# Optimization experiments

Measured on AMD Instinct MI355X. Metric: run time of the kernel, lower is better.

## Reference

```python
import jax, jax.numpy as jnp
import numpy as np

WIN, SIGMA = 11, 1.5
C1, C2, EPS = 0.01 ** 2, 0.03 ** 2, 1e-8


def _gauss_window(win=WIN, sigma=SIGMA):
    coords = jnp.arange(win, dtype=jnp.float32) - (win - 1) / 2
    g = jnp.exp(-coords ** 2 / (2 * sigma ** 2))
    g = g / g.sum()
    return (g[:, None] * g[None, :])[None, None, :, :]


def setup_inputs() -> dict:
    key = jax.random.key(0)
    k1, k2 = jax.random.split(key)
    N, C, H, W = 32, 1, 512, 512
    x = jax.random.uniform(k1, (N, C, H, W), dtype=jnp.float32)
    y = jax.random.uniform(k2, (N, C, H, W), dtype=jnp.float32)
    w = _gauss_window()
    return {"x": x, "y": y, "w": w}


def _conv(x, w):
    pad = w.shape[-1] // 2
    return jax.lax.conv_general_dilated(
        x, w, window_strides=(1, 1), padding=[(pad, pad), (pad, pad)],
        dimension_numbers=("NCHW", "OIHW", "NCHW"))


def reference(x, y, w):
    w = w.astype(x.dtype)
    n = x.shape[0]
    # One fused conv over all five planes stacked on the batch dim.
    stacked = jnp.concatenate([x, y, x * x, y * y, x * y], axis=0)
    conv = _conv(stacked, w)
    mu_x, mu_y, ex2, ey2, exy = (conv[i * n:(i + 1) * n] for i in range(5))
    mu_x2, mu_y2, mu_xy = mu_x ** 2, mu_y ** 2, mu_x * mu_y
    sig_x2 = ex2 - mu_x2
    sig_y2 = ey2 - mu_y2
    sig_xy = exy - mu_xy
    num = (2 * mu_xy + C1) * (2 * sig_xy + C2)
    den = (mu_x2 + mu_y2 + C1) * (sig_x2 + sig_y2 + C2)
    return jnp.clip(num / (den + EPS), 0.0, 1.0).mean()
```

## Files before the change

### kernel.cpp

```cpp
#include <hip/hip_runtime.h>


#define IMG_H 512
#define IMG_W 512
#define NIMG  32
#define TW    128
#define RROWS 64
#define NBANDS (IMG_W / TW)
#define NCHUNK (IMG_H / RROWS)

#define C1F  1.0e-4f
#define C2F  9.0e-4f
#define EPSF 1.0e-8f

__global__ __launch_bounds__(TW) void ssim_kernel(
    const float* __restrict__ xg, const float* __restrict__ yg,
    const float* __restrict__ wg, float* __restrict__ out)
{
    const int t     = threadIdx.x;
    const int band  = blockIdx.x;
    const int chunk = blockIdx.y;
    const int img   = blockIdx.z;
    const int c0 = band * TW;
    const int r0 = chunk * RROWS;
    const float* xb = xg + (size_t)img * (IMG_H * IMG_W);
    const float* yb = yg + (size_t)img * (IMG_H * IMG_W);

    __shared__ float gS[11];
    __shared__ float bufX[2][TW + 16];
    __shared__ float bufY[2][TW + 16];
    __shared__ float wredS[2];

    if (t < 11) {
        float s = 0.f;
        #pragma unroll
        for (int j = 0; j < 11; ++j) s += wg[t * 11 + j];
        gS[t] = s;
    }
    __syncthreads();
    float g[11];
    #pragma unroll
    for (int k = 0; k < 11; ++k) g[k] = gS[k];

    const int colA = c0 + t;
    const int  b2     = (t < 5) ? t : (TW + t);
    const int  colB   = c0 - 5 + b2;
    const bool hasB   = (t < 10);
    const bool colBok = hasB && ((unsigned)colB < IMG_W);

    float vx[11], vy[11], vs[11], vd[11];

    {
        int rcur = r0 - 5;
        bool rok = ((unsigned)rcur < IMG_H);
        (void)rok;
    }
    float lxA, lyA, lxB, lyB;
    {
        int rcur = r0 - 5;
        bool rv = ((unsigned)rcur < IMG_H);
        const float* xr = xb + rcur * IMG_W;
        const float* yr = yb + rcur * IMG_W;
        lxA = rv ? xr[colA] : 0.f;
        lyA = rv ? yr[colA] : 0.f;
        lxB = (rv && colBok) ? xr[colB] : 0.f;
        lyB = (rv && colBok) ? yr[colB] : 0.f;
    }

    float acc = 0.f;

    for (int ii = 0; ii < 77; ii += 11) {
        #pragma unroll
        for (int s = 0; s < 11; ++s) {
            const int i = ii + s;
            if (i < RROWS + 10) {
                const int pb = i & 1;
                bufX[pb][5 + t] = lxA;
                bufY[pb][5 + t] = lyA;
                if (hasB) {
                    bufX[pb][b2] = lxB;
                    bufY[pb][b2] = lyB;
                }
                __syncthreads();

                {
                    int rn = r0 - 4 + i;
                    bool rv = ((unsigned)rn < IMG_H);
                    const float* xr = xb + rn * IMG_W;
                    const float* yr = yb + rn * IMG_W;
                    lxA = rv ? xr[colA] : 0.f;
                    lyA = rv ? yr[colA] : 0.f;
                    lxB = (rv && colBok) ? xr[colB] : 0.f;
                    lyB = (rv && colBok) ? yr[colB] : 0.f;
                }

                float hx = 0.f, hy = 0.f, hs2 = 0.f, hd2 = 0.f;
                #pragma unroll
                for (int k = 0; k < 11; ++k) {
                    float xv = bufX[pb][t + k];
                    float yv = bufY[pb][t + k];
                    hx = fmaf(g[k], xv, hx);
                    hy = fmaf(g[k], yv, hy);
                    float sv = xv + yv;
                    float dv = xv - yv;
                    hs2 = fmaf(g[k], sv * sv, hs2);
                    hd2 = fmaf(g[k], dv * dv, hd2);
                }
                vx[s] = hx; vy[s] = hy; vs[s] = hs2; vd[s] = hd2;

                if (i >= 10) {
                    float mx = 0.f, my = 0.f, ms = 0.f, md = 0.f;
                    #pragma unroll
                    for (int j = 0; j < 11; ++j) {
                        const int sl = (s + 1 + j) % 11;
                        mx = fmaf(g[j], vx[sl], mx);
                        my = fmaf(g[j], vy[sl], my);
                        ms = fmaf(g[j], vs[sl], ms);
                        md = fmaf(g[j], vd[sl], md);
                    }
                    float mux2 = mx * mx, muy2 = my * my, muxy = mx * my;
                    float a    = mux2 + muy2;
                    float esum = 0.5f  * (ms + md);
                    float exy  = 0.25f * (ms - md);
                    float sxy  = exy  - muxy;
                    float ssum = esum - a;
                    float num  = fmaf(2.f, muxy, C1F) * fmaf(2.f, sxy, C2F);
                    float den  = (a + C1F) * (ssum + C2F);
                    float v = num * __builtin_amdgcn_rcpf(den + EPSF);
                    v = fminf(fmaxf(v, 0.f), 1.f);
                    acc += v;
                }
            }
        }
    }

    #pragma unroll
    for (int off = 32; off > 0; off >>= 1)
        acc += __shfl_down(acc, off, 64);
    if ((t & 63) == 0) wredS[t >> 6] = acc;
    __syncthreads();
    if (t == 0) {
        float tot = wredS[0] + wredS[1];
        atomicAdd(out, tot * (1.0f / (float)((size_t)NIMG * IMG_H * IMG_W)));
    }
}

extern "C" void kernel_launch(void* const* d_in, const int* in_sizes, int n_in,
                              void* d_out, int out_size, void* d_ws, size_t ws_size,
                              hipStream_t stream) {
    const float* x = (const float*)d_in[0];
    const float* y = (const float*)d_in[1];
    const float* w = (const float*)d_in[2];
    float* out = (float*)d_out;

    hipMemsetAsync(out, 0, sizeof(float), stream);

    dim3 grid(NBANDS, NCHUNK, NIMG);
    ssim_kernel<<<grid, dim3(TW), 0, stream>>>(x, y, w, out);
}
```

Measured before the change: 136.3 us.

## Compute four output columns per lane with float4 register windows, drop shared memory

Each 64-lane block now handles a 256-column band over 16 rows. Each lane computes four adjacent outputs from a 20-float register window it loads directly with float4 reads, so the LDS staging and per-row __syncthreads are gone. The second-moment planes become x²+y² and xy instead of (x+y)² and (x−y)², which saves the 0.5/0.25 rescale. The costs are redundant halo loads (5 float4 per lane for 4 outputs), much higher register pressure from 11x4x4 row buffers, and smaller row chunks, so a larger share of each block's reads are halo rows.

```diff
diff --git a/kernel.cpp b/kernel.cpp
--- a/kernel.cpp
+++ b/kernel.cpp
@@ -4,131 +4,125 @@
 #define IMG_H 512
 #define IMG_W 512
 #define NIMG  32
-#define TW    128
-#define RROWS 64
-#define NBANDS (IMG_W / TW)
-#define NCHUNK (IMG_H / RROWS)
+#define M     4
+#define RROWS 16
+#define ITERS (RROWS + 10)
+#define NB4   (IMG_W / 4)
 
 #define C1F  1.0e-4f
 #define C2F  9.0e-4f
 #define EPSF 1.0e-8f
 
-__global__ __launch_bounds__(TW) void ssim_kernel(
+__global__ __launch_bounds__(64, 2) void ssim_kernel(
     const float* __restrict__ xg, const float* __restrict__ yg,
     const float* __restrict__ wg, float* __restrict__ out)
 {
-    const int t     = threadIdx.x;
-    const int band  = blockIdx.x;
-    const int chunk = blockIdx.y;
-    const int img   = blockIdx.z;
-    const int c0 = band * TW;
-    const int r0 = chunk * RROWS;
+    const int lane = threadIdx.x;
+    const int band = blockIdx.x;
+    const int chnk = blockIdx.y;
+    const int img  = blockIdx.z;
+    const int r0   = chnk * RROWS;
+    const int fb0  = band * 64 + lane - 2;
+
     const float* xb = xg + (size_t)img * (IMG_H * IMG_W);
     const float* yb = yg + (size_t)img * (IMG_H * IMG_W);
 
-    __shared__ float gS[11];
-    __shared__ float bufX[2][TW + 16];
-    __shared__ float bufY[2][TW + 16];
-    __shared__ float wredS[2];
-
-    if (t < 11) {
-        float s = 0.f;
+    float rs = 0.f;
+    if (lane < 11) {
         #pragma unroll
-        for (int j = 0; j < 11; ++j) s += wg[t * 11 + j];
-        gS[t] = s;
+        for (int j = 0; j < 11; ++j) rs += wg[lane * 11 + j];
     }
-    __syncthreads();
     float g[11];
     #pragma unroll
-    for (int k = 0; k < 11; ++k) g[k] = gS[k];
-
-    const int colA = c0 + t;
-    const int  b2     = (t < 5) ? t : (TW + t);
-    const int  colB   = c0 - 5 + b2;
-    const bool hasB   = (t < 10);
-    const bool colBok = hasB && ((unsigned)colB < IMG_W);
-
-    float vx[11], vy[11], vs[11], vd[11];
-
-    {
-        int rcur = r0 - 5;
-        bool rok = ((unsigned)rcur < IMG_H);
-        (void)rok;
-    }
-    float lxA, lyA, lxB, lyB;
-    {
-        int rcur = r0 - 5;
-        bool rv = ((unsigned)rcur < IMG_H);
-        const float* xr = xb + rcur * IMG_W;
-        const float* yr = yb + rcur * IMG_W;
-        lxA = rv ? xr[colA] : 0.f;
-        lyA = rv ? yr[colA] : 0.f;
-        lxB = (rv && colBok) ? xr[colB] : 0.f;
-        lyB = (rv && colBok) ? yr[colB] : 0.f;
+    for (int k = 0; k < 11; ++k) {
+        int gi = __shfl(__float_as_int(rs), k, 64);
+        g[k] = __int_as_float(__builtin_amdgcn_readfirstlane(gi));
     }
 
+    float rx[11][M], ry[11][M], rp[11][M], rq[11][M];
+
+    const float4 z4 = make_float4(0.f, 0.f, 0.f, 0.f);
     float acc = 0.f;
 
-    for (int ii = 0; ii < 77; ii += 11) {
+    for (int ii = 0; ii < 33; ii += 11) {
         #pragma unroll
         for (int s = 0; s < 11; ++s) {
             const int i = ii + s;
-            if (i < RROWS + 10) {
-                const int pb = i & 1;
-                bufX[pb][5 + t] = lxA;
-                bufY[pb][5 + t] = lyA;
-                if (hasB) {
-                    bufX[pb][b2] = lxB;
-                    bufY[pb][b2] = lyB;
-                }
-                __syncthreads();
-
-                {
-                    int rn = r0 - 4 + i;
-                    bool rv = ((unsigned)rn < IMG_H);
-                    const float* xr = xb + rn * IMG_W;
-                    const float* yr = yb + rn * IMG_W;
-                    lxA = rv ? xr[colA] : 0.f;
-                    lyA = rv ? yr[colA] : 0.f;
-                    lxB = (rv && colBok) ? xr[colB] : 0.f;
-                    lyB = (rv && colBok) ? yr[colB] : 0.f;
+            if (i < ITERS) {
+                const int r = r0 - 5 + i;
+                float4 xv[5], yv[5];
+                if ((unsigned)r < IMG_H) {
+                    const float4* xr4 = (const float4*)(xb + (size_t)r * IMG_W);
+                    const float4* yr4 = (const float4*)(yb + (size_t)r * IMG_W);
+                    #pragma unroll
+                    for (int k = 0; k < 5; ++k) {
+                        const int fb = fb0 + k;
+                        const bool ok = ((unsigned)fb < NB4);
+                        xv[k] = ok ? xr4[fb] : z4;
+                        yv[k] = ok ? yr4[fb] : z4;
+                    }
+                } else {
+                    #pragma unroll
+                    for (int k = 0; k < 5; ++k) { xv[k] = z4; yv[k] = z4; }
                 }
 
-                float hx = 0.f, hy = 0.f, hs2 = 0.f, hd2 = 0.f;
+                float xw[20], yw[20];
                 #pragma unroll
-                for (int k = 0; k < 11; ++k) {
-                    float xv = bufX[pb][t + k];
-                    float yv = bufY[pb][t + k];
-                    hx = fmaf(g[k], xv, hx);
-                    hy = fmaf(g[k], yv, hy);
-                    float sv = xv + yv;
-                    float dv = xv - yv;
-                    hs2 = fmaf(g[k], sv * sv, hs2);
-                    hd2 = fmaf(g[k], dv * dv, hd2);
+                for (int k = 0; k < 5; ++k) {
+                    xw[4*k+0] = xv[k].x; xw[4*k+1] = xv[k].y;
+                    xw[4*k+2] = xv[k].z; xw[4*k+3] = xv[k].w;
+                    yw[4*k+0] = yv[k].x; yw[4*k+1] = yv[k].y;
+                    yw[4*k+2] = yv[k].z; yw[4*k+3] = yv[k].w;
                 }
-                vx[s] = hx; vy[s] = hy; vs[s] = hs2; vd[s] = hd2;
+
+                float hx[M] = {0,0,0,0}, hy[M] = {0,0,0,0};
+                float hp[M] = {0,0,0,0}, hq[M] = {0,0,0,0};
+                #pragma unroll
+                for (int e = 3; e <= 16; ++e) {
+                    const float xe = xw[e], ye = yw[e];
+                    const float pe = fmaf(xe, xe, ye * ye);
+                    const float qe = xe * ye;
+                    const int jlo = (e - 13 > 0) ? (e - 13) : 0;
+                    const int jhi = (e - 3 < M - 1) ? (e - 3) : (M - 1);
+                    #pragma unroll
+                    for (int j = jlo; j <= jhi; ++j) {
+                        const float gk = g[e - 3 - j];
+                        hx[j] = fmaf(gk, xe, hx[j]);
+                        hy[j] = fmaf(gk, ye, hy[j]);
+                        hp[j] = fmaf(gk, pe, hp[j]);
+                        hq[j] = fmaf(gk, qe, hq[j]);
+                    }
+                }
+                #pragma unroll
+                for (int j = 0; j < M; ++j) {
+                    rx[s][j] = hx[j]; ry[s][j] = hy[j];
+                    rp[s][j] = hp[j]; rq[s][j] = hq[j];
+                }
 
                 if (i >= 10) {
-                    float mx = 0.f, my = 0.f, ms = 0.f, md = 0.f;
                     #pragma unroll
-                    for (int j = 0; j < 11; ++j) {
-                        const int sl = (s + 1 + j) % 11;
-                        mx = fmaf(g[j], vx[sl], mx);
-                        my = fmaf(g[j], vy[sl], my);
-                        ms = fmaf(g[j], vs[sl], ms);
-                        md = fmaf(g[j], vd[sl], md);
+                    for (int j = 0; j < M; ++j) {
+                        float mx = 0.f, my = 0.f, mp = 0.f, mq = 0.f;
+                        #pragma unroll
+                        for (int t = 0; t < 11; ++t) {
+                            const int sl = (s + 1 + t) % 11;
+                            mx = fmaf(g[t], rx[sl][j], mx);
+                            my = fmaf(g[t], ry[sl][j], my);
+                            mp = fmaf(g[t], rp[sl][j], mp);
+                            mq = fmaf(g[t], rq[sl][j], mq);
+                        }
+                        const float mux2 = mx * mx;
+                        const float muy2 = my * my;
+                        const float muxy = mx * my;
+                        const float a    = mux2 + muy2;
+                        const float sxy  = mq - muxy;
+                        const float ssum = mp - a;
+                        const float num  = fmaf(2.f, muxy, C1F) * fmaf(2.f, sxy, C2F);
+                        const float den  = (a + C1F) * (ssum + C2F);
+                        float v = num * __builtin_amdgcn_rcpf(den + EPSF);
+                        v = fminf(fmaxf(v, 0.f), 1.f);
+                        acc += v;
                     }
-                    float mux2 = mx * mx, muy2 = my * my, muxy = mx * my;
-                    float a    = mux2 + muy2;
-                    float esum = 0.5f  * (ms + md);
-                    float exy  = 0.25f * (ms - md);
-                    float sxy  = exy  - muxy;
-                    float ssum = esum - a;
-                    float num  = fmaf(2.f, muxy, C1F) * fmaf(2.f, sxy, C2F);
-                    float den  = (a + C1F) * (ssum + C2F);
-                    float v = num * __builtin_amdgcn_rcpf(den + EPSF);
-                    v = fminf(fmaxf(v, 0.f), 1.f);
-                    acc += v;
                 }
             }
         }
@@ -137,12 +131,8 @@
     #pragma unroll
     for (int off = 32; off > 0; off >>= 1)
         acc += __shfl_down(acc, off, 64);
-    if ((t & 63) == 0) wredS[t >> 6] = acc;
-    __syncthreads();
-    if (t == 0) {
-        float tot = wredS[0] + wredS[1];
-        atomicAdd(out, tot * (1.0f / (float)((size_t)NIMG * IMG_H * IMG_W)));
-    }
+    if (lane == 0)
+        atomicAdd(out, acc * (1.0f / (float)((size_t)NIMG * IMG_H * IMG_W)));
 }
 
 extern "C" void kernel_launch(void* const* d_in, const int* in_sizes, int n_in,
@@ -155,6 +145,6 @@
 
     hipMemsetAsync(out, 0, sizeof(float), stream);
 
-    dim3 grid(NBANDS, NCHUNK, NIMG);
-    ssim_kernel<<<grid, dim3(TW), 0, stream>>>(x, y, w, out);
+    dim3 grid(IMG_W / (64 * M), IMG_H / RROWS, NIMG);
+    ssim_kernel<<<grid, dim3(64), 0, stream>>>(x, y, w, out);
 }
```

Result: slower. 179.7 us (+31.9%).

## Precompute per-pixel products into float4 LDS and halve row chunk size

Applied to the files above, without the earlier changes.

Each pixel is now staged once in shared memory as a float4 holding x, y, x²+y² and x·y. The horizontal pass then does a single vector LDS read and four FMAs per tap, instead of two scalar reads plus recomputing sum and difference squares at every tap. The row chunk per block is cut from 64 to 32, which doubles the grid and the parallelism but raises the halo-row overhead from 10/64 to 10/32. Gaussian weights are now shared with wave shuffles instead of a shared-memory write and barrier, and an extra barrier is added before the final reduction.

```diff
diff --git a/kernel.cpp b/kernel.cpp
--- a/kernel.cpp
+++ b/kernel.cpp
@@ -5,9 +5,9 @@
 #define IMG_W 512
 #define NIMG  32
 #define TW    128
-#define RROWS 64
-#define NBANDS (IMG_W / TW)
-#define NCHUNK (IMG_H / RROWS)
+#define RROWS 32
+#define ITERS (RROWS + 10)
+#define LDSW  (TW + 10)
 
 #define C1F  1.0e-4f
 #define C2F  9.0e-4f
@@ -17,30 +17,33 @@
     const float* __restrict__ xg, const float* __restrict__ yg,
     const float* __restrict__ wg, float* __restrict__ out)
 {
-    const int t     = threadIdx.x;
-    const int band  = blockIdx.x;
-    const int chunk = blockIdx.y;
-    const int img   = blockIdx.z;
-    const int c0 = band * TW;
-    const int r0 = chunk * RROWS;
+    const int t    = threadIdx.x;
+    const int band = blockIdx.x;
+    const int chnk = blockIdx.y;
+    const int img  = blockIdx.z;
+    const int c0   = band * TW;
+    const int r0   = chnk * RROWS;
+
     const float* xb = xg + (size_t)img * (IMG_H * IMG_W);
     const float* yb = yg + (size_t)img * (IMG_H * IMG_W);
 
-    __shared__ float gS[11];
-    __shared__ float bufX[2][TW + 16];
-    __shared__ float bufY[2][TW + 16];
+    __shared__ float4 sq[2][LDSW];
     __shared__ float wredS[2];
 
-    if (t < 11) {
-        float s = 0.f;
-        #pragma unroll
-        for (int j = 0; j < 11; ++j) s += wg[t * 11 + j];
-        gS[t] = s;
+    float rs = 0.f;
+    {
+        const int lane = t & 63;
+        if (lane < 11) {
+            #pragma unroll
+            for (int j = 0; j < 11; ++j) rs += wg[lane * 11 + j];
+        }
     }
-    __syncthreads();
     float g[11];
     #pragma unroll
-    for (int k = 0; k < 11; ++k) g[k] = gS[k];
+    for (int k = 0; k < 11; ++k) {
+        int gi = __shfl(__float_as_int(rs), k, 64);
+        g[k] = __int_as_float(__builtin_amdgcn_readfirstlane(gi));
+    }
 
     const int colA = c0 + t;
     const int  b2     = (t < 5) ? t : (TW + t);
@@ -48,19 +51,14 @@
     const bool hasB   = (t < 10);
     const bool colBok = hasB && ((unsigned)colB < IMG_W);
 
-    float vx[11], vy[11], vs[11], vd[11];
+    float rx[11], ry[11], rp[11], rq[11];
 
-    {
-        int rcur = r0 - 5;
-        bool rok = ((unsigned)rcur < IMG_H);
-        (void)rok;
-    }
     float lxA, lyA, lxB, lyB;
     {
-        int rcur = r0 - 5;
-        bool rv = ((unsigned)rcur < IMG_H);
-        const float* xr = xb + rcur * IMG_W;
-        const float* yr = yb + rcur * IMG_W;
+        const int r = r0 - 5;
+        const bool rv = ((unsigned)r < IMG_H);
+        const float* xr = xb + (size_t)r * IMG_W;
+        const float* yr = yb + (size_t)r * IMG_W;
         lxA = rv ? xr[colA] : 0.f;
         lyA = rv ? yr[colA] : 0.f;
         lxB = (rv && colBok) ? xr[colB] : 0.f;
@@ -69,66 +67,69 @@
 
     float acc = 0.f;
 
-    for (int ii = 0; ii < 77; ii += 11) {
+    for (int ii = 0; ii < 44; ii += 11) {
         #pragma unroll
         for (int s = 0; s < 11; ++s) {
             const int i = ii + s;
-            if (i < RROWS + 10) {
+            if (i < ITERS) {
                 const int pb = i & 1;
-                bufX[pb][5 + t] = lxA;
-                bufY[pb][5 + t] = lyA;
-                if (hasB) {
-                    bufX[pb][b2] = lxB;
-                    bufY[pb][b2] = lyB;
+                {
+                    float4 v;
+                    v.x = lxA; v.y = lyA;
+                    v.z = fmaf(lxA, lxA, lyA * lyA);
+                    v.w = lxA * lyA;
+                    sq[pb][5 + t] = v;
+                    if (hasB) {
+                        float4 h;
+                        h.x = lxB; h.y = lyB;
+                        h.z = fmaf(lxB, lxB, lyB * lyB);
+                        h.w = lxB * lyB;
+                        sq[pb][b2] = h;
+                    }
                 }
                 __syncthreads();
 
                 {
-                    int rn = r0 - 4 + i;
-                    bool rv = ((unsigned)rn < IMG_H);
-                    const float* xr = xb + rn * IMG_W;
-                    const float* yr = yb + rn * IMG_W;
+                    const int r = r0 - 4 + i;
+                    const bool rv = ((unsigned)r < IMG_H);
+                    const float* xr = xb + (size_t)r * IMG_W;
+                    const float* yr = yb + (size_t)r * IMG_W;
                     lxA = rv ? xr[colA] : 0.f;
                     lyA = rv ? yr[colA] : 0.f;
                     lxB = (rv && colBok) ? xr[colB] : 0.f;
                     lyB = (rv && colBok) ? yr[colB] : 0.f;
                 }
 
-                float hx = 0.f, hy = 0.f, hs2 = 0.f, hd2 = 0.f;
+                float hx = 0.f, hy = 0.f, hp = 0.f, hq = 0.f;
                 #pragma unroll
                 for (int k = 0; k < 11; ++k) {
-                    float xv = bufX[pb][t + k];
-                    float yv = bufY[pb][t + k];
-                    hx = fmaf(g[k], xv, hx);
-                    hy = fmaf(g[k], yv, hy);
-                    float sv = xv + yv;
-                    float dv = xv - yv;
-                    hs2 = fmaf(g[k], sv * sv, hs2);
-                    hd2 = fmaf(g[k], dv * dv, hd2);
+                    const float4 w = sq[pb][t + k];
+                    hx = fmaf(g[k], w.x, hx);
+                    hy = fmaf(g[k], w.y, hy);
+                    hp = fmaf(g[k], w.z, hp);
+                    hq = fmaf(g[k], w.w, hq);
                 }
-                vx[s] = hx; vy[s] = hy; vs[s] = hs2; vd[s] = hd2;
+                rx[s] = hx; ry[s] = hy; rp[s] = hp; rq[s] = hq;
 
                 if (i >= 10) {
-                    float mx = 0.f, my = 0.f, ms = 0.f, md = 0.f;
+                    float mx = 0.f, my = 0.f, mp = 0.f, mq = 0.f;
                     #pragma unroll
                     for (int j = 0; j < 11; ++j) {
                         const int sl = (s + 1 + j) % 11;
-                        mx = fmaf(g[j], vx[sl], mx);
-                        my = fmaf(g[j], vy[sl], my);
-                        ms = fmaf(g[j], vs[sl], ms);
-                        md = fmaf(g[j], vd[sl], md);
+                        mx = fmaf(g[j], rx[sl], mx);
+                        my = fmaf(g[j], ry[sl], my);
+                        mp = fmaf(g[j], rp[sl], mp);
+                        mq = fmaf(g[j], rq[sl], mq);
                     }
-                    float mux2 = mx * mx, muy2 = my * my, muxy = mx * my;
-                    float a    = mux2 + muy2;
-                    float esum = 0.5f  * (ms + md);
-                    float exy  = 0.25f * (ms - md);
-                    float sxy  = exy  - muxy;
-                    float ssum = esum - a;
-                    float num  = fmaf(2.f, muxy, C1F) * fmaf(2.f, sxy, C2F);
-                    float den  = (a + C1F) * (ssum + C2F);
+                    const float mux2 = mx * mx, muy2 = my * my;
+                    const float muxy = mx * my;
+                    const float a    = mux2 + muy2;
+                    const float sxy  = mq - muxy;
+                    const float ssum = mp - a;
+                    const float num  = fmaf(2.f, muxy, C1F) * fmaf(2.f, sxy, C2F);
+                    const float den  = (a + C1F) * (ssum + C2F);
                     float v = num * __builtin_amdgcn_rcpf(den + EPSF);
-                    v = fminf(fmaxf(v, 0.f), 1.f);
-                    acc += v;
+                    acc += fminf(fmaxf(v, 0.f), 1.f);
                 }
             }
         }
@@ -137,10 +138,11 @@
     #pragma unroll
     for (int off = 32; off > 0; off >>= 1)
         acc += __shfl_down(acc, off, 64);
+    __syncthreads();
     if ((t & 63) == 0) wredS[t >> 6] = acc;
     __syncthreads();
     if (t == 0) {
-        float tot = wredS[0] + wredS[1];
+        const float tot = wredS[0] + wredS[1];
         atomicAdd(out, tot * (1.0f / (float)((size_t)NIMG * IMG_H * IMG_W)));
     }
 }
@@ -155,6 +157,6 @@
 
     hipMemsetAsync(out, 0, sizeof(float), stream);
 
-    dim3 grid(NBANDS, NCHUNK, NIMG);
+    dim3 grid(IMG_W / TW, IMG_H / RROWS, NIMG);
     ssim_kernel<<<grid, dim3(TW), 0, stream>>>(x, y, w, out);
 }
```

Measured after the change: 132.5 us. 2.8% less time.
